# Optimization experiments

Measured on AMD Instinct MI355X. Metric: run time of the kernel, lower is better.

## Reference

```python
import jax, jax.numpy as jnp
import numpy as np

HEADS = 8
DHEAD = 64
A_SCALE = 8.0  # cosine-attention logit scale (a=8 in source)
ROPE_BASE = 10000.0


def _mp_weight(w, centered):
    # Magnitude-preserving (EDM2-style) weight: optional zero-mean over fan-in,
    # unit-norm per output row, scaled by 1/sqrt(fan_in).
    if centered:
        w = w - w.mean(axis=1, keepdims=True)
    w = w / (jnp.linalg.norm(w, axis=1, keepdims=True) + 1e-8)
    return w / jnp.sqrt(jnp.asarray(w.shape[1], w.dtype))


def _rope_cos_sin(Hs, Ws, d, dtype=jnp.float32):
    # 2D axial RoPE: first d/4 rotation pairs encode row position, last d/4 column position.
    quarter = d // 4
    freqs = 1.0 / (ROPE_BASE ** (jnp.arange(quarter, dtype=dtype) / quarter))  # [d/4]
    ah = jnp.arange(Hs, dtype=dtype)[:, None] * freqs                          # [H, d/4]
    aw = jnp.arange(Ws, dtype=dtype)[:, None] * freqs                          # [W, d/4]
    ang = jnp.concatenate([
        jnp.broadcast_to(ah[:, None, :], (Hs, Ws, quarter)),
        jnp.broadcast_to(aw[None, :, :], (Hs, Ws, quarter)),
    ], axis=-1).reshape(Hs * Ws, d // 2)                                       # [L, d/2]
    return jnp.cos(ang), jnp.sin(ang)


def _apply_rope(t, cos, sin):
    # t: [N, h, L, d]; rotate interleaved pairs.
    x1, x2 = t[..., 0::2], t[..., 1::2]
    r1 = x1 * cos - x2 * sin
    r2 = x1 * sin + x2 * cos
    return jnp.stack([r1, r2], axis=-1).reshape(t.shape)


def setup_inputs() -> dict:
    key = jax.random.key(0)
    ks = jax.random.split(key, 8)
    N, C, Hs, Ws = 8, 256, 32, 32
    E, Hc = 512, 512
    return {
        "x": jax.random.normal(ks[0], (N, C, Hs, Ws), jnp.float32),
        "w": jax.random.normal(ks[1], (N, E), jnp.float32),
        "InputGain": jax.random.uniform(ks[2], (3 * Hc,), jnp.float32),
        "ResidualGain": jax.random.uniform(ks[3], (C,), jnp.float32),
        "qkv_w": jax.random.normal(ks[4], (3 * Hc, C), jnp.float32),
        "qkv_b": jnp.zeros((3 * Hc,), jnp.float32),
        "mod_w": jax.random.normal(ks[5], (E, C), jnp.float32) / jnp.sqrt(512.0),
        "proj_w": jax.random.normal(ks[6], (C, Hc), jnp.float32),
        "sinks": jnp.zeros((HEADS,), jnp.float32),
    }


def reference(x, w, InputGain, ResidualGain, qkv_w, qkv_b, mod_w, proj_w, sinks):
    N, C, Hs, Ws = x.shape
    L = Hs * Ws
    Hc = qkv_w.shape[0] // 3

    # --- fused QKV: style-modulated, biased, centered 1x1 conv with per-out-channel gain ---
    style = w @ mod_w + 1.0                                   # [N, C]
    Wq = _mp_weight(qkv_w, centered=True)                     # [3Hc, C]
    xm = x * style[:, :, None, None]
    y = jnp.einsum('nchw,oc->nohw', xm, Wq)
    y = (y + qkv_b[None, :, None, None]) * InputGain[None, :, None, None]  # [N, 3Hc, H, W]

    # --- split heads, flatten space: [N, h, L, d] ---
    y = y.reshape(N, 3, HEADS, DHEAD, L)
    q = jnp.transpose(y[:, 0], (0, 1, 3, 2))
    k = jnp.transpose(y[:, 1], (0, 1, 3, 2))
    v = jnp.transpose(y[:, 2], (0, 1, 3, 2))

    # --- 2D RoPE on q, k ---
    cos, sin = _rope_cos_sin(Hs, Ws, DHEAD, x.dtype)
    q = _apply_rope(q, cos, sin)
    k = _apply_rope(k, cos, sin)

    # --- cosine attention with per-head sink logit ---
    qn = q / (jnp.linalg.norm(q, axis=-1, keepdims=True) + 1e-8)
    kn = k / (jnp.linalg.norm(k, axis=-1, keepdims=True) + 1e-8)
    logits = A_SCALE * jnp.einsum('nhld,nhmd->nhlm', qn, kn)  # [N, h, L, L]
    sink = jnp.broadcast_to(sinks[None, :, None, None], (N, HEADS, L, 1))
    probs = jax.nn.softmax(jnp.concatenate([logits, sink], axis=-1), axis=-1)[..., :L]
    o = jnp.einsum('nhlm,nhmd->nhld', probs, v)               # [N, h, L, d]

    # --- merge heads back to map, centered 1x1 projection with per-out-channel gain ---
    o = jnp.transpose(o, (0, 1, 3, 2)).reshape(N, Hc, Hs, Ws)
    Wp = _mp_weight(proj_w, centered=True) * ResidualGain[:, None]  # [C, Hc]
    out = jnp.einsum('nchw,oc->nohw', o, Wp)
    return x + out
```

## Files before the change

### kernel.cpp

```cpp
#include <hip/hip_runtime.h>
#include <hip/hip_bf16.h>
#include <math.h>

#define NN 8
#define CC 256
#define LL 1024
#define EE 512
#define HEADS 8
#define DH 64

#define OFF_STYLE   0u
#define OFF_BIAS    2048u
#define OFF_COS     3584u
#define OFF_SIN     36352u
#define OFF_WQB     69120u
#define OFF_WPB     265728u
#define OFF_XMT     331264u
#define OFF_Q       1379840u
#define OFF_K       3476992u
#define OFF_V       5574144u
#define OFF_O       7671296u

typedef __bf16 bf16x8 __attribute__((ext_vector_type(8)));
typedef __bf16 bf16x4 __attribute__((ext_vector_type(4)));
typedef short s16x4 __attribute__((ext_vector_type(4)));
typedef float f32x4 __attribute__((ext_vector_type(4)));

__global__ __launch_bounds__(256) void k_style(const float* __restrict__ w,
                                               const float* __restrict__ mod_w,
                                               float* __restrict__ style) {
    int n  = blockIdx.x >> 2;
    int cg = blockIdx.x & 3;
    int wv = threadIdx.x >> 6, lane = threadIdx.x & 63;
    int c = cg * 64 + lane;
    __shared__ float red[4][64];
    float acc = 0.f;
    #pragma unroll 8
    for (int e = wv * 128; e < wv * 128 + 128; ++e)
        acc += w[n * EE + e] * mod_w[e * CC + c];
    red[wv][lane] = acc;
    __syncthreads();
    if (wv == 0)
        style[n * CC + c] = red[0][lane] + red[1][lane] + red[2][lane] + red[3][lane] + 1.0f;
}

__global__ __launch_bounds__(256) void k_prep_wq(const float* __restrict__ qkv_w,
                                                 const float* __restrict__ gain,
                                                 const float* __restrict__ bias,
                                                 __hip_bfloat16* __restrict__ wqb,
                                                 float* __restrict__ biasg) {
    int wv = threadIdx.x >> 6, lane = threadIdx.x & 63;
    int o = blockIdx.x * 4 + wv;
    float4 v = *reinterpret_cast<const float4*>(qkv_w + o * CC + lane * 4);
    float s = v.x + v.y + v.z + v.w;
    #pragma unroll
    for (int off = 1; off < 64; off <<= 1) s += __shfl_xor(s, off);
    float mean = s * (1.0f / 256.0f);
    float c0 = v.x - mean, c1 = v.y - mean, c2 = v.z - mean, c3 = v.w - mean;
    float ss = c0 * c0 + c1 * c1 + c2 * c2 + c3 * c3;
    #pragma unroll
    for (int off = 1; off < 64; off <<= 1) ss += __shfl_xor(ss, off);
    float g = gain[o];
    float scale = g / ((sqrtf(ss) + 1e-8f) * 16.0f);
    bf16x4 outv;
    outv[0] = (__bf16)(c0 * scale); outv[1] = (__bf16)(c1 * scale);
    outv[2] = (__bf16)(c2 * scale); outv[3] = (__bf16)(c3 * scale);
    *reinterpret_cast<bf16x4*>((__bf16*)wqb + o * CC + lane * 4) = outv;
    if (lane == 0) biasg[o] = bias[o] * g;
}

__global__ __launch_bounds__(256) void k_prep_wp(const float* __restrict__ proj_w,
                                                 const float* __restrict__ rgain,
                                                 __hip_bfloat16* __restrict__ wpb) {
    int wv = threadIdx.x >> 6, lane = threadIdx.x & 63;
    int r = blockIdx.x * 4 + wv;
    const float* p = proj_w + r * 512 + lane * 8;
    float4 v0 = *reinterpret_cast<const float4*>(p);
    float4 v1 = *reinterpret_cast<const float4*>(p + 4);
    float s = v0.x + v0.y + v0.z + v0.w + v1.x + v1.y + v1.z + v1.w;
    #pragma unroll
    for (int off = 1; off < 64; off <<= 1) s += __shfl_xor(s, off);
    float mean = s * (1.0f / 512.0f);
    float c[8] = {v0.x - mean, v0.y - mean, v0.z - mean, v0.w - mean,
                  v1.x - mean, v1.y - mean, v1.z - mean, v1.w - mean};
    float ss = 0.f;
    #pragma unroll
    for (int i = 0; i < 8; ++i) ss += c[i] * c[i];
    #pragma unroll
    for (int off = 1; off < 64; off <<= 1) ss += __shfl_xor(ss, off);
    float scale = rgain[r] / ((sqrtf(ss) + 1e-8f) * 22.62741699796952f);
    bf16x8 outv;
    #pragma unroll
    for (int i = 0; i < 8; ++i) outv[i] = (__bf16)(c[i] * scale);
    *reinterpret_cast<bf16x8*>((__bf16*)wpb + r * 512 + lane * 8) = outv;
}

__global__ __launch_bounds__(256) void k_rope(float* __restrict__ cosT, float* __restrict__ sinT) {
    int idx = blockIdx.x * 256 + threadIdx.x;
    int l = idx >> 4, j = idx & 15;
    int hh = l >> 5, ww = l & 31;
    float f = exp2f(-(float)j * 0.8304820238941836f);
    float s1, c1, s2, c2;
    __sincosf((float)hh * f, &s1, &c1);
    __sincosf((float)ww * f, &s2, &c2);
    cosT[l * 32 + j]      = c1;
    sinT[l * 32 + j]      = s1;
    cosT[l * 32 + 16 + j] = c2;
    sinT[l * 32 + 16 + j] = s2;
}

__global__ __launch_bounds__(256) void k_xm(const float* __restrict__ x,
                                            const float* __restrict__ style,
                                            __hip_bfloat16* __restrict__ xmT) {
    int lb = blockIdx.x;
    int cb = blockIdx.y;
    int n  = blockIdx.z;
    int t = threadIdx.x;
    __shared__ float tile[64][68];
    int r = t >> 2, q = t & 3;
    float st = style[n * CC + cb * 64 + r];
    const float* xp = x + (size_t)n * (CC * LL) + (size_t)(cb * 64 + r) * LL + lb * 64 + q * 16;
    #pragma unroll
    for (int i = 0; i < 4; ++i) {
        float4 v = *reinterpret_cast<const float4*>(xp + i * 4);
        tile[r][q * 16 + i * 4 + 0] = v.x * st;
        tile[r][q * 16 + i * 4 + 1] = v.y * st;
        tile[r][q * 16 + i * 4 + 2] = v.z * st;
        tile[r][q * 16 + i * 4 + 3] = v.w * st;
    }
    __syncthreads();
    __hip_bfloat16 outv[16];
    #pragma unroll
    for (int i = 0; i < 16; ++i)
        outv[i] = __float2bfloat16(tile[q * 16 + i][r]);
    __hip_bfloat16* dst = xmT + (size_t)n * (LL * CC) + (size_t)(lb * 64 + r) * CC + cb * 64 + q * 16;
    *reinterpret_cast<bf16x8*>(dst)     = *reinterpret_cast<bf16x8*>(&outv[0]);
    *reinterpret_cast<bf16x8*>(dst + 8) = *reinterpret_cast<bf16x8*>(&outv[8]);
}

__global__ __launch_bounds__(256) void k_qkv3(const __hip_bfloat16* __restrict__ wqb,
                                              const __hip_bfloat16* __restrict__ xmT,
// ... 41 lines not shown
    __syncthreads();

    f32x4 acc[4][4] = {};
    int cur = 0;
    for (int t = 0; t < 4; ++t) {
        if (t < 3) {
            int kt1 = (t + 1) * 64;
            #pragma unroll
            for (int i = 0; i < 4; ++i) {
                ar[i] = *reinterpret_cast<const bf16x8*>(Agl + (size_t)srow[i] * CC + kt1 + scol);
                br[i] = *reinterpret_cast<const bf16x8*>(Bgl + (size_t)srow[i] * CC + kt1 + scol);
            }
        }
        const __hip_bfloat16* At = &smem[cur * 8192];
        const __hip_bfloat16* Bt = &smem[16384 + cur * 8192];
        #pragma unroll
        for (int kk = 0; kk < 2; ++kk) {
            int col = (kk * 32 + g * 8) ^ ((r16 & 7) << 3);
            bf16x8 a[4], b[4];
            #pragma unroll
            for (int m = 0; m < 4; ++m)
                a[m] = *reinterpret_cast<const bf16x8*>(&At[(wr * 64 + m * 16 + r16) * 64 + col]);
            #pragma unroll
            for (int nn = 0; nn < 4; ++nn)
                b[nn] = *reinterpret_cast<const bf16x8*>(&Bt[(wc * 64 + nn * 16 + r16) * 64 + col]);
            __builtin_amdgcn_s_setprio(1);
            #pragma unroll
            for (int m = 0; m < 4; ++m)
                #pragma unroll
                for (int nn = 0; nn < 4; ++nn)
                    acc[m][nn] = __builtin_amdgcn_mfma_f32_16x16x32_bf16(a[m], b[nn], acc[m][nn], 0, 0, 0);
            __builtin_amdgcn_s_setprio(0);
        }
        __syncthreads();
        if (t < 3) {
            #pragma unroll
            for (int i = 0; i < 4; ++i) {
                *reinterpret_cast<bf16x8*>(&smem[(cur ^ 1) * 8192 + srow[i] * 64 + sswz[i]]) = ar[i];
                *reinterpret_cast<bf16x8*>(&smem[16384 + (cur ^ 1) * 8192 + srow[i] * 64 + sswz[i]]) = br[i];
            }
            __syncthreads();
        }
        cur ^= 1;
    }
    __syncthreads();

    __hip_bfloat16 (*sw)[64][72] = reinterpret_cast<__hip_bfloat16 (*)[64][72]>(smem);

    float bg[4][4];
    #pragma unroll
    for (int m = 0; m < 4; ++m)
        #pragma unroll
        for (int reg = 0; reg < 4; ++reg)
            bg[m][reg] = biasg[o0 + m * 16 + 4 * g + reg];

    size_t head = (size_t)(n * 8 + h);

    if (part < 2) {
        __hip_bfloat16* dst = (part == 0) ? qb : kb;
        #pragma unroll
        for (int nn = 0; nn < 4; ++nn) {
            int l = l0 + nn * 16 + r16;
            float rv[4][4];
            float ss = 0.f;
            #pragma unroll
            for (int m = 0; m < 4; ++m) {
                int j0 = m * 8 + g * 2;
                float cA = cosT[l * 32 + j0],     sA = sinT[l * 32 + j0];
                float cB = cosT[l * 32 + j0 + 1], sB = sinT[l * 32 + j0 + 1];
                float x0 = acc[m][nn][0] + bg[m][0];
                float x1 = acc[m][nn][1] + bg[m][1];
                float x2 = acc[m][nn][2] + bg[m][2];
                float x3 = acc[m][nn][3] + bg[m][3];
                rv[m][0] = x0 * cA - x1 * sA;
                rv[m][1] = x0 * sA + x1 * cA;
                rv[m][2] = x2 * cB - x3 * sB;
                rv[m][3] = x2 * sB + x3 * cB;
                ss += rv[m][0] * rv[m][0] + rv[m][1] * rv[m][1] +
// ... 10 lines not shown
                        __float2bfloat16(rv[m][reg] * inv);
        }
        #pragma unroll
        for (int it = 0; it < 8; ++it) {
            int idx = lane + it * 64;
            int ll = idx >> 3, ch = idx & 7;
            bf16x8 v = *reinterpret_cast<bf16x8*>(&sw[wid][ll][ch * 8]);
            *reinterpret_cast<bf16x8*>(dst + (head * LL + l0 + ll) * DH + ch * 8) = v;
        }
    } else {
        #pragma unroll
        for (int nn = 0; nn < 4; ++nn)
            #pragma unroll
            for (int m = 0; m < 4; ++m)
                #pragma unroll
                for (int reg = 0; reg < 4; ++reg)
                    sw[wid][m * 16 + 4 * g + reg][nn * 16 + r16] =
                        __float2bfloat16(acc[m][nn][reg] + bg[m][reg]);
        #pragma unroll
        for (int it = 0; it < 8; ++it) {
            int idx = lane + it * 64;
            int dd = idx >> 3, ch = idx & 7;
            bf16x8 v = *reinterpret_cast<bf16x8*>(&sw[wid][dd][ch * 8]);
            *reinterpret_cast<bf16x8*>(vt + (head * DH + dd) * LL + l0 + ch * 8) = v;
        }
    }
}

__global__ __launch_bounds__(256) void k_attn_mfma(
    const __hip_bfloat16* __restrict__ qb, const __hip_bfloat16* __restrict__ kb,
    const __hip_bfloat16* __restrict__ vt, const float* __restrict__ sinks,
    __hip_bfloat16* __restrict__ ob) {
    int bid = blockIdx.x;
    int swz = (bid & 7) * 64 + (bid >> 3);
    int n    = swz >> 6;
    int h    = (swz >> 3) & 7;
    int qblk = swz & 7;
    int tid  = threadIdx.x;
    int wid  = tid >> 6, lane = tid & 63;
    int g = lane >> 4, r16 = lane & 15;

    size_t head = (size_t)(n * 8 + h);
    const __hip_bfloat16* Q = qb + head * (size_t)(LL * DH);
    const __hip_bfloat16* K = kb + head * (size_t)(LL * DH);
    const __hip_bfloat16* V = vt + head * (size_t)(DH * LL);
    __hip_bfloat16* O = ob + (size_t)n * (LL * 512) + h * 64;

    int q0 = qblk * 128 + wid * 32;

    __shared__ __hip_bfloat16 kls[2][64][64];
    __shared__ __hip_bfloat16 vls[2][64][64];

    const int cl0 = tid >> 3,        cd0 = (tid & 7) * 8;
    const int cl1 = (tid + 256) >> 3, cd1 = (tid & 7) * 8;
    const int ksw0 = cd0 ^ ((cl0 & 7) << 3);
    const int ksw1 = cd1 ^ ((cl1 & 7) << 3);

    bf16x8 qf[2][2];
    #pragma unroll
    for (int qm = 0; qm < 2; ++qm)
        #pragma unroll
        for (int dc = 0; dc < 2; ++dc)
            qf[qm][dc] = *reinterpret_cast<const bf16x8*>(
                Q + (size_t)(q0 + qm * 16 + r16) * DH + dc * 32 + g * 8);

    float snk = sinks[h];
    float m = fmaxf(8.0f, snk);
    const float c1 = 8.0f * 1.44269504f;
    const float c0 = -m * 1.44269504f;

    f32x4 oacc[2][4];
    #pragma unroll
    for (int qm = 0; qm < 2; ++qm)
        #pragma unroll
        for (int dn = 0; dn < 4; ++dn)
            oacc[qm][dn] = (f32x4){0.f, 0.f, 0.f, 0.f};
    float ssum[2] = {0.f, 0.f};

    bf16x8 kr0, kr1, vr0, vr1;
    kr0 = *reinterpret_cast<const bf16x8*>(K + (size_t)cl0 * DH + cd0);
    kr1 = *reinterpret_cast<const bf16x8*>(K + (size_t)cl1 * DH + cd1);
    vr0 = *reinterpret_cast<const bf16x8*>(V + (size_t)cl0 * LL + cd0);
    vr1 = *reinterpret_cast<const bf16x8*>(V + (size_t)cl1 * LL + cd1);
    *reinterpret_cast<bf16x8*>(&kls[0][cl0][ksw0]) = kr0;
    *reinterpret_cast<bf16x8*>(&kls[0][cl1][ksw1]) = kr1;
    *reinterpret_cast<bf16x8*>(&vls[0][cl0][ksw0]) = vr0;
    *reinterpret_cast<bf16x8*>(&vls[0][cl1][ksw1]) = vr1;
    __syncthreads();

    int cur = 0;
    for (int t = 0; t < 16; ++t) {
        if (t < 15) {
            int kt1 = t * 64 + 64;
            kr0 = *reinterpret_cast<const bf16x8*>(K + (size_t)(kt1 + cl0) * DH + cd0);
            kr1 = *reinterpret_cast<const bf16x8*>(K + (size_t)(kt1 + cl1) * DH + cd1);
            vr0 = *reinterpret_cast<const bf16x8*>(V + (size_t)cl0 * LL + kt1 + cd0);
            vr1 = *reinterpret_cast<const bf16x8*>(V + (size_t)cl1 * LL + kt1 + cd1);
        }
        f32x4 sacc[2][4];
        #pragma unroll
        for (int qm = 0; qm < 2; ++qm)
            #pragma unroll
            for (int kn = 0; kn < 4; ++kn)
                sacc[qm][kn] = (f32x4){0.f, 0.f, 0.f, 0.f};
        __builtin_amdgcn_s_setprio(1);
        #pragma unroll
        for (int kn = 0; kn < 4; ++kn) {
            #pragma unroll
            for (int dc = 0; dc < 2; ++dc) {
                bf16x8 kf = *reinterpret_cast<const bf16x8*>(
                    &kls[cur][kn * 16 + r16][(dc * 32 + g * 8) ^ ((r16 & 7) << 3)]);
                #pragma unroll
                for (int qm = 0; qm < 2; ++qm)
                    sacc[qm][kn] = __builtin_amdgcn_mfma_f32_16x16x32_bf16(
                        kf, qf[qm][dc], sacc[qm][kn], 0, 0, 0);
            }
        }
        __builtin_amdgcn_s_setprio(0);
        #pragma unroll
        for (int kn = 0; kn < 4; ++kn) {
            s16x4 pa[2];
            #pragma unroll
            for (int qm = 0; qm < 2; ++qm) {
                float p0 = exp2f(fmaf(sacc[qm][kn][0], c1, c0));
                float p1 = exp2f(fmaf(sacc[qm][kn][1], c1, c0));
                float p2 = exp2f(fmaf(sacc[qm][kn][2], c1, c0));
                float p3 = exp2f(fmaf(sacc[qm][kn][3], c1, c0));
                ssum[qm] += p0 + p1 + p2 + p3;
                bf16x4 pb;
                pb[0] = (__bf16)p0; pb[1] = (__bf16)p1;
                pb[2] = (__bf16)p2; pb[3] = (__bf16)p3;
                pa[qm] = __builtin_bit_cast(s16x4, pb);
            }
            __builtin_amdgcn_s_setprio(1);
            #pragma unroll
            for (int dn = 0; dn < 4; ++dn) {
                s16x4 vb = *reinterpret_cast<const s16x4*>(
                    &vls[cur][dn * 16 + r16][(kn * 16 + g * 4) ^ ((r16 & 7) << 3)]);
                #pragma unroll
                for (int qm = 0; qm < 2; ++qm)
                    oacc[qm][dn] = __builtin_amdgcn_mfma_f32_16x16x16bf16_1k(
                        pa[qm], vb, oacc[qm][dn], 0, 0, 0);
            }
            __builtin_amdgcn_s_setprio(0);
        }
        __syncthreads();
        if (t < 15) {
            *reinterpret_cast<bf16x8*>(&kls[cur ^ 1][cl0][ksw0]) = kr0;
            *reinterpret_cast<bf16x8*>(&kls[cur ^ 1][cl1][ksw1]) = kr1;
            *reinterpret_cast<bf16x8*>(&vls[cur ^ 1][cl0][ksw0]) = vr0;
            *reinterpret_cast<bf16x8*>(&vls[cur ^ 1][cl1][ksw1]) = vr1;
            __syncthreads();
        }
        cur ^= 1;
    }

    float sink_e = exp2f((snk - m) * 1.44269504f);
    float inv[2];
    #pragma unroll
    for (int qm = 0; qm < 2; ++qm) {
        float s = ssum[qm];
        s += __shfl_xor(s, 16);
        s += __shfl_xor(s, 32);
        inv[qm] = 1.0f / (s + sink_e);
    }
    #pragma unroll
    for (int qm = 0; qm < 2; ++qm) {
        #pragma unroll
        for (int reg = 0; reg < 4; ++reg) {
            float invq = __shfl(inv[qm], 4 * g + reg);
            #pragma unroll
            for (int dn = 0; dn < 4; ++dn)
                O[(size_t)(q0 + qm * 16 + 4 * g + reg) * 512 + dn * 16 + r16] =
                    __float2bfloat16(oacc[qm][dn][reg] * invq);
        }
    }
}

__global__ __launch_bounds__(256) void k_proj3(const __hip_bfloat16* __restrict__ wpb,
                                               const __hip_bfloat16* __restrict__ ob,
                                               const float* __restrict__ x,
                                               float* __restrict__ out) {
    int lb = blockIdx.x;
    int cb = blockIdx.y;
    int n  = blockIdx.z;
    int tid = threadIdx.x;
    int wid = tid >> 6, lane = tid & 63;
    int wr = wid >> 1, wc = wid & 1;
    int g = lane >> 4, r16 = lane & 15;

    int c0 = cb * 64 + wr * 32;
    int l0 = lb * 128 + wc * 64;

    __shared__ __hip_bfloat16 smem[24576];

    const int arow[2] = {tid >> 3, (tid + 256) >> 3};
    const int brow[4] = {tid >> 3, (tid + 256) >> 3, (tid + 512) >> 3, (tid + 768) >> 3};
    const int scol = (tid & 7) * 8;
    int aswz[2], bswz[4];
    #pragma unroll
    for (int i = 0; i < 2; ++i) aswz[i] = scol ^ ((arow[i] & 7) << 3);
    #pragma unroll
    for (int i = 0; i < 4; ++i) bswz[i] = scol ^ ((brow[i] & 7) << 3);

    const __hip_bfloat16* Agl = wpb + (size_t)(cb * 64) * 512;
    const __hip_bfloat16* Bgl = ob + (size_t)n * (LL * 512) + (size_t)(lb * 128) * 512;

    bf16x8 ar[2], br[4];
// ... 13 lines not shown

    f32x4 acc[2][4] = {};
    int cur = 0;
    for (int t = 0; t < 8; ++t) {
        if (t < 7) {
            int kt1 = (t + 1) * 64;
            #pragma unroll
            for (int i = 0; i < 2; ++i)
                ar[i] = *reinterpret_cast<const bf16x8*>(Agl + (size_t)arow[i] * 512 + kt1 + scol);
            #pragma unroll
            for (int i = 0; i < 4; ++i)
                br[i] = *reinterpret_cast<const bf16x8*>(Bgl + (size_t)brow[i] * 512 + kt1 + scol);
        }
        const __hip_bfloat16* At = &smem[cur * 4096];
        const __hip_bfloat16* Bt = &smem[8192 + cur * 8192];
        #pragma unroll
        for (int kk = 0; kk < 2; ++kk) {
            int col = (kk * 32 + g * 8) ^ ((r16 & 7) << 3);
            bf16x8 a[2], b[4];
            #pragma unroll
            for (int m = 0; m < 2; ++m)
                a[m] = *reinterpret_cast<const bf16x8*>(&At[(wr * 32 + m * 16 + r16) * 64 + col]);
            #pragma unroll
            for (int nn = 0; nn < 4; ++nn)
                b[nn] = *reinterpret_cast<const bf16x8*>(&Bt[(wc * 64 + nn * 16 + r16) * 64 + col]);
            __builtin_amdgcn_s_setprio(1);
            #pragma unroll
            for (int m = 0; m < 2; ++m)
                #pragma unroll
                for (int nn = 0; nn < 4; ++nn)
                    acc[m][nn] = __builtin_amdgcn_mfma_f32_16x16x32_bf16(a[m], b[nn], acc[m][nn], 0, 0, 0);
            __builtin_amdgcn_s_setprio(0);
        }
        __syncthreads();
        if (t < 7) {
            #pragma unroll
            for (int i = 0; i < 2; ++i)
                *reinterpret_cast<bf16x8*>(&smem[(cur ^ 1) * 4096 + arow[i] * 64 + aswz[i]]) = ar[i];
            #pragma unroll
            for (int i = 0; i < 4; ++i)
                *reinterpret_cast<bf16x8*>(&smem[8192 + (cur ^ 1) * 8192 + brow[i] * 64 + bswz[i]]) = br[i];
            __syncthreads();
        }
        cur ^= 1;
    }

    #pragma unroll
    for (int m = 0; m < 2; ++m) {
        #pragma unroll
        for (int reg = 0; reg < 4; ++reg) {
            int c = c0 + m * 16 + 4 * g + reg;
            #pragma unroll
            for (int nn = 0; nn < 4; ++nn) {
                int l = l0 + nn * 16 + r16;
                size_t idx = (size_t)n * (CC * LL) + (size_t)c * LL + l;
                out[idx] = x[idx] + acc[m][nn][reg];
            }
        }
    }
}

extern "C" void kernel_launch(void* const* d_in, const int* in_sizes, int n_in,
                              void* d_out, int out_size, void* d_ws, size_t ws_size,
                              hipStream_t stream) {
    const float* x       = (const float*)d_in[0];
    const float* w       = (const float*)d_in[1];
    const float* igain   = (const float*)d_in[2];
    const float* rgain   = (const float*)d_in[3];
    const float* qkv_w   = (const float*)d_in[4];
    const float* qkv_b   = (const float*)d_in[5];
    const float* mod_w   = (const float*)d_in[6];
    const float* proj_w  = (const float*)d_in[7];
    const float* sinks   = (const float*)d_in[8];
    float* out = (float*)d_out;
    float* ws  = (float*)d_ws;

    float* style = ws + OFF_STYLE;
    float* biasg = ws + OFF_BIAS;
    float* cosT  = ws + OFF_COS;
    float* sinT  = ws + OFF_SIN;
    __hip_bfloat16* wqb = (__hip_bfloat16*)(ws + OFF_WQB);
    __hip_bfloat16* wpb = (__hip_bfloat16*)(ws + OFF_WPB);
    __hip_bfloat16* xmT = (__hip_bfloat16*)(ws + OFF_XMT);
    __hip_bfloat16* qb  = (__hip_bfloat16*)(ws + OFF_Q);
    __hip_bfloat16* kb  = (__hip_bfloat16*)(ws + OFF_K);
    __hip_bfloat16* vt  = (__hip_bfloat16*)(ws + OFF_V);
    __hip_bfloat16* obuf = (__hip_bfloat16*)(ws + OFF_O);

    k_style<<<32, 256, 0, stream>>>(w, mod_w, style);
    k_prep_wq<<<384, 256, 0, stream>>>(qkv_w, igain, qkv_b, wqb, biasg);
    k_prep_wp<<<64, 256, 0, stream>>>(proj_w, rgain, wpb);
    k_rope<<<64, 256, 0, stream>>>(cosT, sinT);
    k_xm<<<dim3(16, 4, NN), 256, 0, stream>>>(x, style, xmT);
    k_qkv3<<<dim3(8, 12, NN), 256, 0, stream>>>(wqb, xmT, biasg, cosT, sinT, qb, kb, vt);
    k_attn_mfma<<<512, 256, 0, stream>>>(qb, kb, vt, sinks, obuf);
    k_proj3<<<dim3(8, 4, NN), 256, 0, stream>>>(wpb, obuf, x, out);
}
```

Measured before the change: 91.79 us.

## Merge prep kernels, halve attention query tile, compute row sums via MFMA

Four small setup kernels (style, qkv weight prep, proj weight prep, rope table) become a single block-dispatched kernel, which removes three launches. The attention kernel now gives each wave 16 query rows instead of 32 and launches 1024 blocks instead of 512, so more blocks are in flight on the GPU. Softmax row sums are accumulated by an extra MFMA against a ones vector, replacing the VALU sums and cross-lane shuffles. In exchange each loaded K/V tile is reused by half as many query rows, so LDS and global K/V traffic per unit of work doubles.

New measurement: 85.55 us. 6.8% less time.

```diff
diff --git a/kernel.cpp b/kernel.cpp
--- a/kernel.cpp
+++ b/kernel.cpp
@@ -26,87 +26,81 @@
 typedef short s16x4 __attribute__((ext_vector_type(4)));
 typedef float f32x4 __attribute__((ext_vector_type(4)));
 
-__global__ __launch_bounds__(256) void k_style(const float* __restrict__ w,
-                                               const float* __restrict__ mod_w,
-                                               float* __restrict__ style) {
-    int n  = blockIdx.x >> 2;
-    int cg = blockIdx.x & 3;
-    int wv = threadIdx.x >> 6, lane = threadIdx.x & 63;
-    int c = cg * 64 + lane;
-    __shared__ float red[4][64];
-    float acc = 0.f;
-    #pragma unroll 8
-    for (int e = wv * 128; e < wv * 128 + 128; ++e)
-        acc += w[n * EE + e] * mod_w[e * CC + c];
-    red[wv][lane] = acc;
-    __syncthreads();
-    if (wv == 0)
-        style[n * CC + c] = red[0][lane] + red[1][lane] + red[2][lane] + red[3][lane] + 1.0f;
-}
-
-__global__ __launch_bounds__(256) void k_prep_wq(const float* __restrict__ qkv_w,
-                                                 const float* __restrict__ gain,
-                                                 const float* __restrict__ bias,
-                                                 __hip_bfloat16* __restrict__ wqb,
-                                                 float* __restrict__ biasg) {
-    int wv = threadIdx.x >> 6, lane = threadIdx.x & 63;
-    int o = blockIdx.x * 4 + wv;
-    float4 v = *reinterpret_cast<const float4*>(qkv_w + o * CC + lane * 4);
-    float s = v.x + v.y + v.z + v.w;
-    #pragma unroll
-    for (int off = 1; off < 64; off <<= 1) s += __shfl_xor(s, off);
-    float mean = s * (1.0f / 256.0f);
-    float c0 = v.x - mean, c1 = v.y - mean, c2 = v.z - mean, c3 = v.w - mean;
-    float ss = c0 * c0 + c1 * c1 + c2 * c2 + c3 * c3;
-    #pragma unroll
-    for (int off = 1; off < 64; off <<= 1) ss += __shfl_xor(ss, off);
-    float g = gain[o];
-    float scale = g / ((sqrtf(ss) + 1e-8f) * 16.0f);
-    bf16x4 outv;
-    outv[0] = (__bf16)(c0 * scale); outv[1] = (__bf16)(c1 * scale);
-    outv[2] = (__bf16)(c2 * scale); outv[3] = (__bf16)(c3 * scale);
-    *reinterpret_cast<bf16x4*>((__bf16*)wqb + o * CC + lane * 4) = outv;
-    if (lane == 0) biasg[o] = bias[o] * g;
-}
-
-__global__ __launch_bounds__(256) void k_prep_wp(const float* __restrict__ proj_w,
-                                                 const float* __restrict__ rgain,
-                                                 __hip_bfloat16* __restrict__ wpb) {
-    int wv = threadIdx.x >> 6, lane = threadIdx.x & 63;
-    int r = blockIdx.x * 4 + wv;
-    const float* p = proj_w + r * 512 + lane * 8;
-    float4 v0 = *reinterpret_cast<const float4*>(p);
-    float4 v1 = *reinterpret_cast<const float4*>(p + 4);
-    float s = v0.x + v0.y + v0.z + v0.w + v1.x + v1.y + v1.z + v1.w;
-    #pragma unroll
-    for (int off = 1; off < 64; off <<= 1) s += __shfl_xor(s, off);
-    float mean = s * (1.0f / 512.0f);
-    float c[8] = {v0.x - mean, v0.y - mean, v0.z - mean, v0.w - mean,
-                  v1.x - mean, v1.y - mean, v1.z - mean, v1.w - mean};
-    float ss = 0.f;
-    #pragma unroll
-    for (int i = 0; i < 8; ++i) ss += c[i] * c[i];
-    #pragma unroll
-    for (int off = 1; off < 64; off <<= 1) ss += __shfl_xor(ss, off);
-    float scale = rgain[r] / ((sqrtf(ss) + 1e-8f) * 22.62741699796952f);
-    bf16x8 outv;
-    #pragma unroll
-    for (int i = 0; i < 8; ++i) outv[i] = (__bf16)(c[i] * scale);
-    *reinterpret_cast<bf16x8*>((__bf16*)wpb + r * 512 + lane * 8) = outv;
-}
-
-__global__ __launch_bounds__(256) void k_rope(float* __restrict__ cosT, float* __restrict__ sinT) {
-    int idx = blockIdx.x * 256 + threadIdx.x;
-    int l = idx >> 4, j = idx & 15;
-    int hh = l >> 5, ww = l & 31;
-    float f = exp2f(-(float)j * 0.8304820238941836f);
-    float s1, c1, s2, c2;
-    __sincosf((float)hh * f, &s1, &c1);
-    __sincosf((float)ww * f, &s2, &c2);
-    cosT[l * 32 + j]      = c1;
-    sinT[l * 32 + j]      = s1;
-    cosT[l * 32 + 16 + j] = c2;
-    sinT[l * 32 + 16 + j] = s2;
+__global__ __launch_bounds__(256) void k_prep(
+    const float* __restrict__ w, const float* __restrict__ mod_w, float* __restrict__ style,
+    const float* __restrict__ qkv_w, const float* __restrict__ gain,
+    const float* __restrict__ bias, __hip_bfloat16* __restrict__ wqb, float* __restrict__ biasg,
+    const float* __restrict__ proj_w, const float* __restrict__ rgain,
+    __hip_bfloat16* __restrict__ wpb,
+    float* __restrict__ cosT, float* __restrict__ sinT) {
+    int bid = blockIdx.x;
+    int t = threadIdx.x;
+    int wv = t >> 6, lane = t & 63;
+    if (bid < 384) {
+        int o = bid * 4 + wv;
+        float4 v = *reinterpret_cast<const float4*>(qkv_w + o * CC + lane * 4);
+        float s = v.x + v.y + v.z + v.w;
+        #pragma unroll
+        for (int off = 1; off < 64; off <<= 1) s += __shfl_xor(s, off);
+        float mean = s * (1.0f / 256.0f);
+        float c0 = v.x - mean, c1 = v.y - mean, c2 = v.z - mean, c3 = v.w - mean;
+        float ss = c0 * c0 + c1 * c1 + c2 * c2 + c3 * c3;
+        #pragma unroll
+        for (int off = 1; off < 64; off <<= 1) ss += __shfl_xor(ss, off);
+        float g = gain[o];
+        float scale = g / ((sqrtf(ss) + 1e-8f) * 16.0f);
+        bf16x4 outv;
+        outv[0] = (__bf16)(c0 * scale); outv[1] = (__bf16)(c1 * scale);
+        outv[2] = (__bf16)(c2 * scale); outv[3] = (__bf16)(c3 * scale);
+        *reinterpret_cast<bf16x4*>((__bf16*)wqb + o * CC + lane * 4) = outv;
+        if (lane == 0) biasg[o] = bias[o] * g;
+    } else if (bid < 448) {
+        int r = (bid - 384) * 4 + wv;
+        const float* p = proj_w + r * 512 + lane * 8;
+        float4 v0 = *reinterpret_cast<const float4*>(p);
+        float4 v1 = *reinterpret_cast<const float4*>(p + 4);
+        float s = v0.x + v0.y + v0.z + v0.w + v1.x + v1.y + v1.z + v1.w;
+        #pragma unroll
+        for (int off = 1; off < 64; off <<= 1) s += __shfl_xor(s, off);
+        float mean = s * (1.0f / 512.0f);
+        float c[8] = {v0.x - mean, v0.y - mean, v0.z - mean, v0.w - mean,
+                      v1.x - mean, v1.y - mean, v1.z - mean, v1.w - mean};
+        float ss = 0.f;
+        #pragma unroll
+        for (int i = 0; i < 8; ++i) ss += c[i] * c[i];
+        #pragma unroll
+        for (int off = 1; off < 64; off <<= 1) ss += __shfl_xor(ss, off);
+        float scale = rgain[r] / ((sqrtf(ss) + 1e-8f) * 22.62741699796952f);
+        bf16x8 outv;
+        #pragma unroll
+        for (int i = 0; i < 8; ++i) outv[i] = (__bf16)(c[i] * scale);
+        *reinterpret_cast<bf16x8*>((__bf16*)wpb + r * 512 + lane * 8) = outv;
+    } else if (bid < 512) {
+        int idx = (bid - 448) * 256 + t;
+        int l = idx >> 4, j = idx & 15;
+        int hh = l >> 5, ww = l & 31;
+        float f = exp2f(-(float)j * 0.8304820238941836f);
+        float s1, c1, s2, c2;
+        __sincosf((float)hh * f, &s1, &c1);
+        __sincosf((float)ww * f, &s2, &c2);
+        cosT[l * 32 + j]      = c1;
+        sinT[l * 32 + j]      = s1;
+        cosT[l * 32 + 16 + j] = c2;
+        sinT[l * 32 + 16 + j] = s2;
+    } else {
+        int b = bid - 512;
+        int n = b >> 2, cg = b & 3;
+        int c = cg * 64 + lane;
+        __shared__ float red[4][64];
+        float acc = 0.f;
+        #pragma unroll 8
+        for (int e = wv * 128; e < wv * 128 + 128; ++e)
+            acc += w[n * EE + e] * mod_w[e * CC + c];
+        red[wv][lane] = acc;
+        __syncthreads();
+        if (wv == 0)
+            style[n * CC + c] = red[0][lane] + red[1][lane] + red[2][lane] + red[3][lane] + 1.0f;
+    }
 }
 
 __global__ __launch_bounds__(256) void k_xm(const float* __restrict__ x,
@@ -302,10 +296,10 @@
     const __hip_bfloat16* __restrict__ vt, const float* __restrict__ sinks,
     __hip_bfloat16* __restrict__ ob) {
     int bid = blockIdx.x;
-    int swz = (bid & 7) * 64 + (bid >> 3);
-    int n    = swz >> 6;
-    int h    = (swz >> 3) & 7;
-    int qblk = swz & 7;
+    int swz = (bid & 7) * 128 + (bid >> 3);
+    int n    = swz >> 7;
+    int h    = (swz >> 4) & 7;
+    int qblk = swz & 15;
     int tid  = threadIdx.x;
     int wid  = tid >> 6, lane = tid & 63;
     int g = lane >> 4, r16 = lane & 15;
@@ -316,7 +310,7 @@
     const __hip_bfloat16* V = vt + head * (size_t)(DH * LL);
     __hip_bfloat16* O = ob + (size_t)n * (LL * 512) + h * 64;
 
-    int q0 = qblk * 128 + wid * 32;
+    int q0 = qblk * 64 + wid * 16;
 
     __shared__ __hip_bfloat16 kls[2][64][64];
     __shared__ __hip_bfloat16 vls[2][64][64];
@@ -326,26 +320,23 @@
     const int ksw0 = cd0 ^ ((cl0 & 7) << 3);
     const int ksw1 = cd1 ^ ((cl1 & 7) << 3);
 
-    bf16x8 qf[2][2];
-    #pragma unroll
-    for (int qm = 0; qm < 2; ++qm)
-        #pragma unroll
-        for (int dc = 0; dc < 2; ++dc)
-            qf[qm][dc] = *reinterpret_cast<const bf16x8*>(
-                Q + (size_t)(q0 + qm * 16 + r16) * DH + dc * 32 + g * 8);
+    bf16x8 qf[2];
+    #pragma unroll
+    for (int dc = 0; dc < 2; ++dc)
+        qf[dc] = *reinterpret_cast<const bf16x8*>(
+            Q + (size_t)(q0 + r16) * DH + dc * 32 + g * 8);
 
     float snk = sinks[h];
     float m = fmaxf(8.0f, snk);
     const float c1 = 8.0f * 1.44269504f;
     const float c0 = -m * 1.44269504f;
 
-    f32x4 oacc[2][4];
-    #pragma unroll
-    for (int qm = 0; qm < 2; ++qm)
-        #pragma unroll
-        for (int dn = 0; dn < 4; ++dn)
-            oacc[qm][dn] = (f32x4){0.f, 0.f, 0.f, 0.f};
-    float ssum[2] = {0.f, 0.f};
+    f32x4 oacc[4];
+    #pragma unroll
+    for (int dn = 0; dn < 4; ++dn)
+        oacc[dn] = (f32x4){0.f, 0.f, 0.f, 0.f};
+    f32x4 osum = (f32x4){0.f, 0.f, 0.f, 0.f};
+    const s16x4 ones = {(short)0x3F80, (short)0x3F80, (short)0x3F80, (short)0x3F80};
 
     bf16x8 kr0, kr1, vr0, vr1;
     kr0 = *reinterpret_cast<const bf16x8*>(K + (size_t)cl0 * DH + cd0);
@@ -367,12 +358,10 @@
             vr0 = *reinterpret_cast<const bf16x8*>(V + (size_t)cl0 * LL + kt1 + cd0);
             vr1 = *reinterpret_cast<const bf16x8*>(V + (size_t)cl1 * LL + kt1 + cd1);
         }
-        f32x4 sacc[2][4];
-        #pragma unroll
-        for (int qm = 0; qm < 2; ++qm)
-            #pragma unroll
-            for (int kn = 0; kn < 4; ++kn)
-                sacc[qm][kn] = (f32x4){0.f, 0.f, 0.f, 0.f};
+        f32x4 sacc[4];
+        #pragma unroll
+        for (int kn = 0; kn < 4; ++kn)
+            sacc[kn] = (f32x4){0.f, 0.f, 0.f, 0.f};
         __builtin_amdgcn_s_setprio(1);
         #pragma unroll
         for (int kn = 0; kn < 4; ++kn) {
@@ -380,37 +369,28 @@
             for (int dc = 0; dc < 2; ++dc) {
                 bf16x8 kf = *reinterpret_cast<const bf16x8*>(
                     &kls[cur][kn * 16 + r16][(dc * 32 + g * 8) ^ ((r16 & 7) << 3)]);
-                #pragma unroll
-                for (int qm = 0; qm < 2; ++qm)
-                    sacc[qm][kn] = __builtin_amdgcn_mfma_f32_16x16x32_bf16(
-                        kf, qf[qm][dc], sacc[qm][kn], 0, 0, 0);
+                sacc[kn] = __builtin_amdgcn_mfma_f32_16x16x32_bf16(
+                    kf, qf[dc], sacc[kn], 0, 0, 0);
             }
         }
         __builtin_amdgcn_s_setprio(0);
         #pragma unroll
         for (int kn = 0; kn < 4; ++kn) {
-            s16x4 pa[2];
-            #pragma unroll
-            for (int qm = 0; qm < 2; ++qm) {
-                float p0 = exp2f(fmaf(sacc[qm][kn][0], c1, c0));
-                float p1 = exp2f(fmaf(sacc[qm][kn][1], c1, c0));
-                float p2 = exp2f(fmaf(sacc[qm][kn][2], c1, c0));
-                float p3 = exp2f(fmaf(sacc[qm][kn][3], c1, c0));
-                ssum[qm] += p0 + p1 + p2 + p3;
-                bf16x4 pb;
-                pb[0] = (__bf16)p0; pb[1] = (__bf16)p1;
-                pb[2] = (__bf16)p2; pb[3] = (__bf16)p3;
-                pa[qm] = __builtin_bit_cast(s16x4, pb);
-            }
+            float p0 = exp2f(fmaf(sacc[kn][0], c1, c0));
+            float p1 = exp2f(fmaf(sacc[kn][1], c1, c0));
+            float p2 = exp2f(fmaf(sacc[kn][2], c1, c0));
+            float p3 = exp2f(fmaf(sacc[kn][3], c1, c0));
+            bf16x4 pb;
+            pb[0] = (__bf16)p0; pb[1] = (__bf16)p1;
+            pb[2] = (__bf16)p2; pb[3] = (__bf16)p3;
+            s16x4 pa = __builtin_bit_cast(s16x4, pb);
             __builtin_amdgcn_s_setprio(1);
+            osum = __builtin_amdgcn_mfma_f32_16x16x16bf16_1k(pa, ones, osum, 0, 0, 0);
             #pragma unroll
             for (int dn = 0; dn < 4; ++dn) {
                 s16x4 vb = *reinterpret_cast<const s16x4*>(
                     &vls[cur][dn * 16 + r16][(kn * 16 + g * 4) ^ ((r16 & 7) << 3)]);
-                #pragma unroll
-                for (int qm = 0; qm < 2; ++qm)
-                    oacc[qm][dn] = __builtin_amdgcn_mfma_f32_16x16x16bf16_1k(
-                        pa[qm], vb, oacc[qm][dn], 0, 0, 0);
+                oacc[dn] = __builtin_amdgcn_mfma_f32_16x16x16bf16_1k(pa, vb, oacc[dn], 0, 0, 0);
             }
             __builtin_amdgcn_s_setprio(0);
         }
@@ -426,24 +406,13 @@
     }
 
     float sink_e = exp2f((snk - m) * 1.44269504f);
-    float inv[2];
-    #pragma unroll
-    for (int qm = 0; qm < 2; ++qm) {
-        float s = ssum[qm];
-        s += __shfl_xor(s, 16);
-        s += __shfl_xor(s, 32);
-        inv[qm] = 1.0f / (s + sink_e);
-    }
-    #pragma unroll
-    for (int qm = 0; qm < 2; ++qm) {
-        #pragma unroll
-        for (int reg = 0; reg < 4; ++reg) {
-            float invq = __shfl(inv[qm], 4 * g + reg);
-            #pragma unroll
-            for (int dn = 0; dn < 4; ++dn)
-                O[(size_t)(q0 + qm * 16 + 4 * g + reg) * 512 + dn * 16 + r16] =
-                    __float2bfloat16(oacc[qm][dn][reg] * invq);
-        }
+    #pragma unroll
+    for (int reg = 0; reg < 4; ++reg) {
+        float invq = 1.0f / (osum[reg] + sink_e);
+        #pragma unroll
+        for (int dn = 0; dn < 4; ++dn)
+            O[(size_t)(q0 + 4 * g + reg) * 512 + dn * 16 + r16] =
+                __float2bfloat16(oacc[dn][reg] * invq);
     }
 }
 
@@ -578,12 +547,10 @@
     __hip_bfloat16* vt  = (__hip_bfloat16*)(ws + OFF_V);
     __hip_bfloat16* obuf = (__hip_bfloat16*)(ws + OFF_O);
 
-    k_style<<<32, 256, 0, stream>>>(w, mod_w, style);
-    k_prep_wq<<<384, 256, 0, stream>>>(qkv_w, igain, qkv_b, wqb, biasg);
-    k_prep_wp<<<64, 256, 0, stream>>>(proj_w, rgain, wpb);
-    k_rope<<<64, 256, 0, stream>>>(cosT, sinT);
+    k_prep<<<544, 256, 0, stream>>>(w, mod_w, style, qkv_w, igain, qkv_b, wqb, biasg,
+                                    proj_w, rgain, wpb, cosT, sinT);
     k_xm<<<dim3(16, 4, NN), 256, 0, stream>>>(x, style, xmT);
     k_qkv3<<<dim3(8, 12, NN), 256, 0, stream>>>(wqb, xmT, biasg, cosT, sinT, qb, kb, vt);
-    k_attn_mfma<<<512, 256, 0, stream>>>(qb, kb, vt, sinks, obuf);
+    k_attn_mfma<<<1024, 256, 0, stream>>>(qb, kb, vt, sinks, obuf);
     k_proj3<<<dim3(8, 4, NN), 256, 0, stream>>>(wpb, obuf, x, out);
 }
```

## Fuse prep kernels, drop barriers, MFMA row sums, and reswizzle V in attention

Applied to the files above, without the earlier changes.

The four small setup kernels (style, qkv weight prep, proj weight prep, RoPE tables) are merged into one launch that branches on block index, removing three launch gaps. In the qkv, attention and projection GEMM loops, the barrier before the double-buffer store and the one after the loop are dropped, leaving one barrier per iteration. That is safe only because the store targets the other buffer. The attention kernel now computes softmax row sums with an extra MFMA against a ones vector instead of scalar adds plus shuffles. V tiles get a finer 4-element XOR swizzle to cut LDS bank conflicts on the s16x4 reads. The cost is split 8-byte LDS stores and a few more MFMAs per tile.

After: 83.63 us. 8.9% less time.

```diff
diff --git a/kernel.cpp b/kernel.cpp
--- a/kernel.cpp
+++ b/kernel.cpp
@@ -24,89 +24,84 @@
 typedef __bf16 bf16x8 __attribute__((ext_vector_type(8)));
 typedef __bf16 bf16x4 __attribute__((ext_vector_type(4)));
 typedef short s16x4 __attribute__((ext_vector_type(4)));
+typedef short s16x8 __attribute__((ext_vector_type(8)));
 typedef float f32x4 __attribute__((ext_vector_type(4)));
 
-__global__ __launch_bounds__(256) void k_style(const float* __restrict__ w,
-                                               const float* __restrict__ mod_w,
-                                               float* __restrict__ style) {
-    int n  = blockIdx.x >> 2;
-    int cg = blockIdx.x & 3;
-    int wv = threadIdx.x >> 6, lane = threadIdx.x & 63;
-    int c = cg * 64 + lane;
-    __shared__ float red[4][64];
-    float acc = 0.f;
-    #pragma unroll 8
-    for (int e = wv * 128; e < wv * 128 + 128; ++e)
-        acc += w[n * EE + e] * mod_w[e * CC + c];
-    red[wv][lane] = acc;
-    __syncthreads();
-    if (wv == 0)
-        style[n * CC + c] = red[0][lane] + red[1][lane] + red[2][lane] + red[3][lane] + 1.0f;
-}
-
-__global__ __launch_bounds__(256) void k_prep_wq(const float* __restrict__ qkv_w,
-                                                 const float* __restrict__ gain,
-                                                 const float* __restrict__ bias,
-                                                 __hip_bfloat16* __restrict__ wqb,
-                                                 float* __restrict__ biasg) {
-    int wv = threadIdx.x >> 6, lane = threadIdx.x & 63;
-    int o = blockIdx.x * 4 + wv;
-    float4 v = *reinterpret_cast<const float4*>(qkv_w + o * CC + lane * 4);
-    float s = v.x + v.y + v.z + v.w;
-    #pragma unroll
-    for (int off = 1; off < 64; off <<= 1) s += __shfl_xor(s, off);
-    float mean = s * (1.0f / 256.0f);
-    float c0 = v.x - mean, c1 = v.y - mean, c2 = v.z - mean, c3 = v.w - mean;
-    float ss = c0 * c0 + c1 * c1 + c2 * c2 + c3 * c3;
-    #pragma unroll
-    for (int off = 1; off < 64; off <<= 1) ss += __shfl_xor(ss, off);
-    float g = gain[o];
-    float scale = g / ((sqrtf(ss) + 1e-8f) * 16.0f);
-    bf16x4 outv;
-    outv[0] = (__bf16)(c0 * scale); outv[1] = (__bf16)(c1 * scale);
-    outv[2] = (__bf16)(c2 * scale); outv[3] = (__bf16)(c3 * scale);
-    *reinterpret_cast<bf16x4*>((__bf16*)wqb + o * CC + lane * 4) = outv;
-    if (lane == 0) biasg[o] = bias[o] * g;
-}
-
-__global__ __launch_bounds__(256) void k_prep_wp(const float* __restrict__ proj_w,
-                                                 const float* __restrict__ rgain,
-                                                 __hip_bfloat16* __restrict__ wpb) {
-    int wv = threadIdx.x >> 6, lane = threadIdx.x & 63;
-    int r = blockIdx.x * 4 + wv;
-    const float* p = proj_w + r * 512 + lane * 8;
-    float4 v0 = *reinterpret_cast<const float4*>(p);
-    float4 v1 = *reinterpret_cast<const float4*>(p + 4);
-    float s = v0.x + v0.y + v0.z + v0.w + v1.x + v1.y + v1.z + v1.w;
-    #pragma unroll
-    for (int off = 1; off < 64; off <<= 1) s += __shfl_xor(s, off);
-    float mean = s * (1.0f / 512.0f);
-    float c[8] = {v0.x - mean, v0.y - mean, v0.z - mean, v0.w - mean,
-                  v1.x - mean, v1.y - mean, v1.z - mean, v1.w - mean};
-    float ss = 0.f;
-    #pragma unroll
-    for (int i = 0; i < 8; ++i) ss += c[i] * c[i];
-    #pragma unroll
-    for (int off = 1; off < 64; off <<= 1) ss += __shfl_xor(ss, off);
-    float scale = rgain[r] / ((sqrtf(ss) + 1e-8f) * 22.62741699796952f);
-    bf16x8 outv;
-    #pragma unroll
-    for (int i = 0; i < 8; ++i) outv[i] = (__bf16)(c[i] * scale);
-    *reinterpret_cast<bf16x8*>((__bf16*)wpb + r * 512 + lane * 8) = outv;
-}
-
-__global__ __launch_bounds__(256) void k_rope(float* __restrict__ cosT, float* __restrict__ sinT) {
-    int idx = blockIdx.x * 256 + threadIdx.x;
-    int l = idx >> 4, j = idx & 15;
-    int hh = l >> 5, ww = l & 31;
-    float f = exp2f(-(float)j * 0.8304820238941836f);
-    float s1, c1, s2, c2;
-    __sincosf((float)hh * f, &s1, &c1);
-    __sincosf((float)ww * f, &s2, &c2);
-    cosT[l * 32 + j]      = c1;
-    sinT[l * 32 + j]      = s1;
-    cosT[l * 32 + 16 + j] = c2;
-    sinT[l * 32 + 16 + j] = s2;
+__global__ __launch_bounds__(256) void k_prep(
+    const float* __restrict__ w, const float* __restrict__ mod_w, float* __restrict__ style,
+    const float* __restrict__ qkv_w, const float* __restrict__ gain,
+    const float* __restrict__ bias, __hip_bfloat16* __restrict__ wqb, float* __restrict__ biasg,
+    const float* __restrict__ proj_w, const float* __restrict__ rgain,
+    __hip_bfloat16* __restrict__ wpb,
+    float* __restrict__ cosT, float* __restrict__ sinT) {
+    int bid = blockIdx.x;
+    int t = threadIdx.x;
+    int wv = t >> 6, lane = t & 63;
+    if (bid < 384) {
+        int o = bid * 4 + wv;
+        float4 v = *reinterpret_cast<const float4*>(qkv_w + o * CC + lane * 4);
+        float s = v.x + v.y + v.z + v.w;
+        #pragma unroll
+        for (int off = 1; off < 64; off <<= 1) s += __shfl_xor(s, off);
+        float mean = s * (1.0f / 256.0f);
+        float c0 = v.x - mean, c1 = v.y - mean, c2 = v.z - mean, c3 = v.w - mean;
+        float ss = c0 * c0 + c1 * c1 + c2 * c2 + c3 * c3;
+        #pragma unroll
+        for (int off = 1; off < 64; off <<= 1) ss += __shfl_xor(ss, off);
+        float g = gain[o];
+        float scale = g / ((sqrtf(ss) + 1e-8f) * 16.0f);
+        bf16x4 outv;
+        outv[0] = (__bf16)(c0 * scale); outv[1] = (__bf16)(c1 * scale);
+        outv[2] = (__bf16)(c2 * scale); outv[3] = (__bf16)(c3 * scale);
+        *reinterpret_cast<bf16x4*>((__bf16*)wqb + o * CC + lane * 4) = outv;
+        if (lane == 0) biasg[o] = bias[o] * g;
+    } else if (bid < 448) {
+        int r = (bid - 384) * 4 + wv;
+        const float* p = proj_w + r * 512 + lane * 8;
+        float4 v0 = *reinterpret_cast<const float4*>(p);
+        float4 v1 = *reinterpret_cast<const float4*>(p + 4);
+        float s = v0.x + v0.y + v0.z + v0.w + v1.x + v1.y + v1.z + v1.w;
+        #pragma unroll
+        for (int off = 1; off < 64; off <<= 1) s += __shfl_xor(s, off);
+        float mean = s * (1.0f / 512.0f);
+        float c[8] = {v0.x - mean, v0.y - mean, v0.z - mean, v0.w - mean,
+                      v1.x - mean, v1.y - mean, v1.z - mean, v1.w - mean};
+        float ss = 0.f;
+        #pragma unroll
+        for (int i = 0; i < 8; ++i) ss += c[i] * c[i];
+        #pragma unroll
+        for (int off = 1; off < 64; off <<= 1) ss += __shfl_xor(ss, off);
+        float scale = rgain[r] / ((sqrtf(ss) + 1e-8f) * 22.62741699796952f);
+        bf16x8 outv;
+        #pragma unroll
+        for (int i = 0; i < 8; ++i) outv[i] = (__bf16)(c[i] * scale);
+        *reinterpret_cast<bf16x8*>((__bf16*)wpb + r * 512 + lane * 8) = outv;
+    } else if (bid < 512) {
+        int idx = (bid - 448) * 256 + t;
+        int l = idx >> 4, j = idx & 15;
+        int hh = l >> 5, ww = l & 31;
+        float f = exp2f(-(float)j * 0.8304820238941836f);
+        float s1, c1, s2, c2;
+        __sincosf((float)hh * f, &s1, &c1);
+        __sincosf((float)ww * f, &s2, &c2);
+        cosT[l * 32 + j]      = c1;
+        sinT[l * 32 + j]      = s1;
+        cosT[l * 32 + 16 + j] = c2;
+        sinT[l * 32 + 16 + j] = s2;
+    } else {
+        int b = bid - 512;
+        int n = b >> 2, cg = b & 3;
+        int c = cg * 64 + lane;
+        __shared__ float red[4][64];
+        float acc = 0.f;
+        #pragma unroll 8
+        for (int e = wv * 128; e < wv * 128 + 128; ++e)
+            acc += w[n * EE + e] * mod_w[e * CC + c];
+        red[wv][lane] = acc;
+        __syncthreads();
+        if (wv == 0)
+            style[n * CC + c] = red[0][lane] + red[1][lane] + red[2][lane] + red[3][lane] + 1.0f;
+    }
 }
 
 __global__ __launch_bounds__(256) void k_xm(const float* __restrict__ x,
@@ -214,18 +209,16 @@
                     acc[m][nn] = __builtin_amdgcn_mfma_f32_16x16x32_bf16(a[m], b[nn], acc[m][nn], 0, 0, 0);
             __builtin_amdgcn_s_setprio(0);
         }
-        __syncthreads();
         if (t < 3) {
             #pragma unroll
             for (int i = 0; i < 4; ++i) {
                 *reinterpret_cast<bf16x8*>(&smem[(cur ^ 1) * 8192 + srow[i] * 64 + sswz[i]]) = ar[i];
                 *reinterpret_cast<bf16x8*>(&smem[16384 + (cur ^ 1) * 8192 + srow[i] * 64 + sswz[i]]) = br[i];
             }
-            __syncthreads();
-        }
+        }
+        __syncthreads();
         cur ^= 1;
     }
-    __syncthreads();
 
     __hip_bfloat16 (*sw)[64][72] = reinterpret_cast<__hip_bfloat16 (*)[64][72]>(smem);
 
@@ -321,10 +314,14 @@
     __shared__ __hip_bfloat16 kls[2][64][64];
     __shared__ __hip_bfloat16 vls[2][64][64];
 
-    const int cl0 = tid >> 3,        cd0 = (tid & 7) * 8;
-    const int cl1 = (tid + 256) >> 3, cd1 = (tid & 7) * 8;
+    const int cl0 = tid >> 3,         cd0 = (tid & 7) * 8;
+    const int cl1 = (tid + 256) >> 3;
     const int ksw0 = cd0 ^ ((cl0 & 7) << 3);
-    const int ksw1 = cd1 ^ ((cl1 & 7) << 3);
+    const int ksw1 = cd0 ^ ((cl1 & 7) << 3);
+    const int vswA0 = cd0       ^ ((cl0 & 15) << 2);
+    const int vswB0 = (cd0 + 4) ^ ((cl0 & 15) << 2);
+    const int vswA1 = cd0       ^ ((cl1 & 15) << 2);
+    const int vswB1 = (cd0 + 4) ^ ((cl1 & 15) << 2);
 
     bf16x8 qf[2][2];
     #pragma unroll
@@ -345,17 +342,26 @@
         #pragma unroll
         for (int dn = 0; dn < 4; ++dn)
             oacc[qm][dn] = (f32x4){0.f, 0.f, 0.f, 0.f};
-    float ssum[2] = {0.f, 0.f};
+    f32x4 osum[2];
+    osum[0] = (f32x4){0.f, 0.f, 0.f, 0.f};
+    osum[1] = (f32x4){0.f, 0.f, 0.f, 0.f};
+    const s16x4 ones = {(short)0x3F80, (short)0x3F80, (short)0x3F80, (short)0x3F80};
 
     bf16x8 kr0, kr1, vr0, vr1;
     kr0 = *reinterpret_cast<const bf16x8*>(K + (size_t)cl0 * DH + cd0);
-    kr1 = *reinterpret_cast<const bf16x8*>(K + (size_t)cl1 * DH + cd1);
+    kr1 = *reinterpret_cast<const bf16x8*>(K + (size_t)cl1 * DH + cd0);
     vr0 = *reinterpret_cast<const bf16x8*>(V + (size_t)cl0 * LL + cd0);
-    vr1 = *reinterpret_cast<const bf16x8*>(V + (size_t)cl1 * LL + cd1);
-    *reinterpret_cast<bf16x8*>(&kls[0][cl0][ksw0]) = kr0;
-    *reinterpret_cast<bf16x8*>(&kls[0][cl1][ksw1]) = kr1;
-    *reinterpret_cast<bf16x8*>(&vls[0][cl0][ksw0]) = vr0;
-    *reinterpret_cast<bf16x8*>(&vls[0][cl1][ksw1]) = vr1;
+    vr1 = *reinterpret_cast<const bf16x8*>(V + (size_t)cl1 * LL + cd0);
+    {
+        *reinterpret_cast<bf16x8*>(&kls[0][cl0][ksw0]) = kr0;
+        *reinterpret_cast<bf16x8*>(&kls[0][cl1][ksw1]) = kr1;
+        s16x8 w0 = __builtin_bit_cast(s16x8, vr0);
+        s16x8 w1 = __builtin_bit_cast(s16x8, vr1);
+        *reinterpret_cast<s16x4*>(&vls[0][cl0][vswA0]) = __builtin_shufflevector(w0, w0, 0, 1, 2, 3);
+        *reinterpret_cast<s16x4*>(&vls[0][cl0][vswB0]) = __builtin_shufflevector(w0, w0, 4, 5, 6, 7);
+        *reinterpret_cast<s16x4*>(&vls[0][cl1][vswA1]) = __builtin_shufflevector(w1, w1, 0, 1, 2, 3);
+        *reinterpret_cast<s16x4*>(&vls[0][cl1][vswB1]) = __builtin_shufflevector(w1, w1, 4, 5, 6, 7);
+    }
     __syncthreads();
 
     int cur = 0;
@@ -363,9 +369,9 @@
         if (t < 15) {
             int kt1 = t * 64 + 64;
             kr0 = *reinterpret_cast<const bf16x8*>(K + (size_t)(kt1 + cl0) * DH + cd0);
-            kr1 = *reinterpret_cast<const bf16x8*>(K + (size_t)(kt1 + cl1) * DH + cd1);
+            kr1 = *reinterpret_cast<const bf16x8*>(K + (size_t)(kt1 + cl1) * DH + cd0);
             vr0 = *reinterpret_cast<const bf16x8*>(V + (size_t)cl0 * LL + kt1 + cd0);
-            vr1 = *reinterpret_cast<const bf16x8*>(V + (size_t)cl1 * LL + kt1 + cd1);
+            vr1 = *reinterpret_cast<const bf16x8*>(V + (size_t)cl1 * LL + kt1 + cd0);
         }
         f32x4 sacc[2][4];
         #pragma unroll
@@ -396,7 +402,6 @@
                 float p1 = exp2f(fmaf(sacc[qm][kn][1], c1, c0));
                 float p2 = exp2f(fmaf(sacc[qm][kn][2], c1, c0));
                 float p3 = exp2f(fmaf(sacc[qm][kn][3], c1, c0));
-                ssum[qm] += p0 + p1 + p2 + p3;
                 bf16x4 pb;
                 pb[0] = (__bf16)p0; pb[1] = (__bf16)p1;
                 pb[2] = (__bf16)p2; pb[3] = (__bf16)p3;
@@ -404,9 +409,12 @@
             }
             __builtin_amdgcn_s_setprio(1);
             #pragma unroll
+            for (int qm = 0; qm < 2; ++qm)
+                osum[qm] = __builtin_amdgcn_mfma_f32_16x16x16bf16_1k(pa[qm], ones, osum[qm], 0, 0, 0);
+            #pragma unroll
             for (int dn = 0; dn < 4; ++dn) {
                 s16x4 vb = *reinterpret_cast<const s16x4*>(
-                    &vls[cur][dn * 16 + r16][(kn * 16 + g * 4) ^ ((r16 & 7) << 3)]);
+                    &vls[cur][dn * 16 + r16][(kn * 16 + g * 4) ^ ((r16 & 15) << 2)]);
                 #pragma unroll
                 for (int qm = 0; qm < 2; ++qm)
                     oacc[qm][dn] = __builtin_amdgcn_mfma_f32_16x16x16bf16_1k(
@@ -414,31 +422,26 @@
             }
             __builtin_amdgcn_s_setprio(0);
         }
-        __syncthreads();
         if (t < 15) {
             *reinterpret_cast<bf16x8*>(&kls[cur ^ 1][cl0][ksw0]) = kr0;
             *reinterpret_cast<bf16x8*>(&kls[cur ^ 1][cl1][ksw1]) = kr1;
-            *reinterpret_cast<bf16x8*>(&vls[cur ^ 1][cl0][ksw0]) = vr0;
-            *reinterpret_cast<bf16x8*>(&vls[cur ^ 1][cl1][ksw1]) = vr1;
-            __syncthreads();
-        }
+            s16x8 w0 = __builtin_bit_cast(s16x8, vr0);
+            s16x8 w1 = __builtin_bit_cast(s16x8, vr1);
+            *reinterpret_cast<s16x4*>(&vls[cur ^ 1][cl0][vswA0]) = __builtin_shufflevector(w0, w0, 0, 1, 2, 3);
+            *reinterpret_cast<s16x4*>(&vls[cur ^ 1][cl0][vswB0]) = __builtin_shufflevector(w0, w0, 4, 5, 6, 7);
+            *reinterpret_cast<s16x4*>(&vls[cur ^ 1][cl1][vswA1]) = __builtin_shufflevector(w1, w1, 0, 1, 2, 3);
+            *reinterpret_cast<s16x4*>(&vls[cur ^ 1][cl1][vswB1]) = __builtin_shufflevector(w1, w1, 4, 5, 6, 7);
+        }
+        __syncthreads();
         cur ^= 1;
     }
 
     float sink_e = exp2f((snk - m) * 1.44269504f);
-    float inv[2];
     #pragma unroll
     for (int qm = 0; qm < 2; ++qm) {
-        float s = ssum[qm];
-        s += __shfl_xor(s, 16);
-        s += __shfl_xor(s, 32);
-        inv[qm] = 1.0f / (s + sink_e);
-    }
-    #pragma unroll
-    for (int qm = 0; qm < 2; ++qm) {
         #pragma unroll
         for (int reg = 0; reg < 4; ++reg) {
-            float invq = __shfl(inv[qm], 4 * g + reg);
+            float invq = 1.0f / (osum[qm][reg] + sink_e);
             #pragma unroll
             for (int dn = 0; dn < 4; ++dn)
                 O[(size_t)(q0 + qm * 16 + 4 * g + reg) * 512 + dn * 16 + r16] =
@@ -523,7 +526,6 @@
                     acc[m][nn] = __builtin_amdgcn_mfma_f32_16x16x32_bf16(a[m], b[nn], acc[m][nn], 0, 0, 0);
             __builtin_amdgcn_s_setprio(0);
         }
-        __syncthreads();
         if (t < 7) {
             #pragma unroll
             for (int i = 0; i < 2; ++i)
@@ -531,8 +533,8 @@
             #pragma unroll
             for (int i = 0; i < 4; ++i)
                 *reinterpret_cast<bf16x8*>(&smem[8192 + (cur ^ 1) * 8192 + brow[i] * 64 + bswz[i]]) = br[i];
-            __syncthreads();
-        }
+        }
+        __syncthreads();
         cur ^= 1;
     }
 
@@ -578,10 +580,8 @@
     __hip_bfloat16* vt  = (__hip_bfloat16*)(ws + OFF_V);
     __hip_bfloat16* obuf = (__hip_bfloat16*)(ws + OFF_O);
 
-    k_style<<<32, 256, 0, stream>>>(w, mod_w, style);
-    k_prep_wq<<<384, 256, 0, stream>>>(qkv_w, igain, qkv_b, wqb, biasg);
-    k_prep_wp<<<64, 256, 0, stream>>>(proj_w, rgain, wpb);
-    k_rope<<<64, 256, 0, stream>>>(cosT, sinT);
+    k_prep<<<544, 256, 0, stream>>>(w, mod_w, style, qkv_w, igain, qkv_b, wqb, biasg,
+                                    proj_w, rgain, wpb, cosT, sinT);
     k_xm<<<dim3(16, 4, NN), 256, 0, stream>>>(x, style, xmT);
     k_qkv3<<<dim3(8, 12, NN), 256, 0, stream>>>(wqb, xmT, biasg, cosT, sinT, qb, kb, vt);
     k_attn_mfma<<<512, 256, 0, stream>>>(qb, kb, vt, sinks, obuf);
```
